# Kernel optimization log

Measured on AMD Instinct MI355X. Metric: run time of the kernel, lower is better.

Reference implementation:

```python
import jax, jax.numpy as jnp
import numpy as np
from jax import lax

B, M, E, H = 16, 64, 256, 256  # batch items, cells per item, n_embedding, n_hidden
S = 4 * M                       # candidate nodes per item (4 per cell)
CLIP = 10.0                     # pointer logit clipping C


def setup_inputs() -> dict:
    key = jax.random.key(0)
    ks = jax.random.split(key, 12)
    sc = 0.05  # keep tanh unsaturated
    return {
        "cell_embed": jax.random.normal(ks[0], (B, S, E), jnp.float32),
        "original_node": jax.random.uniform(ks[1], (B, S, 4), jnp.float32),
        "maze": jnp.zeros((B, 4, 4), jnp.int32),  # unused by the math (torch code builds .tolist() but never uses it)
        "num_cell": M,
        "costs": jax.random.uniform(ks[2], (B, S), jnp.float32),
        "init_w": jax.random.uniform(ks[3], (2 * E,), jnp.float32, -1.0, 1.0),
        "Whc": jax.random.normal(ks[4], (E, E), jnp.float32) * sc,
        "bhc": jax.random.normal(ks[5], (E,), jnp.float32) * sc,
        "Wv": jax.random.normal(ks[6], (2 * E, E), jnp.float32) * sc,
        "bv": jax.random.normal(ks[7], (E,), jnp.float32) * sc,
        "Wq": jax.random.normal(ks[8], (E, H), jnp.float32) * sc,
        "Wk": jax.random.normal(ks[9], (E, H), jnp.float32) * sc,
        "vptr": jax.random.normal(ks[10], (H,), jnp.float32) * sc,
    }


def reference(cell_embed, original_node, maze, num_cell, costs, init_w, Whc, bhc, Wv, bv, Wq, Wk, vptr):
    key = jax.random.key(42)
    bkeys = jax.random.split(key, cell_embed.shape[0])

    def decode_one(emb, node, cost, bkey):
        # emb: [S, E], node: [S, 4], cost: [S]
        h_bar = emb.mean(0) @ Whc + bhc            # h_context_embed(mean)
        k_proj = emb @ Wk                          # [S, H], hoisted out of loop
        q0 = h_bar + init_w @ Wv + bv              # query at step 0

        def step(carry, i):
            query, mask, init_h, st_idx = carry
            # pointer attention: u_j = v^T tanh(Wq q + Wk k_j); logits = C*tanh(u)
            u = jnp.tanh(query @ Wq + k_proj) @ vptr          # [S]
            lg = jnp.where(mask > 0, -1e9, CLIP * jnp.tanh(u))
            idx = jax.random.categorical(jax.random.fold_in(bkey, i), lg)
            logp = jax.nn.log_softmax(lg)[idx]
            # reward: exit point of previous node -> entry point of chosen node, plus internal costs
            ext = jnp.sqrt(jnp.sum((node[idx, :2] - node[st_idx, 2:]) ** 2))
            reward = jnp.where(i > 0, ext + cost[st_idx] + cost[idx], 0.0)
            # mask the whole 4-node cell containing idx, plus idx itself
            mask = lax.dynamic_update_slice(mask, jnp.ones((4,), mask.dtype), (4 * (idx // 4),))
            mask = mask.at[idx].set(1)
            h = emb[idx]                                       # selected node embedding
            init_h = jnp.where(i == 0, h, init_h)
            query = h_bar + jnp.concatenate([init_h, h]) @ Wv + bv
            return (query, mask, init_h, idx), (logp, reward, idx)

        carry0 = (q0, jnp.zeros((emb.shape[0],), jnp.int32),
                  jnp.zeros((emb.shape[1],), emb.dtype), jnp.int32(0))
        _, (logps, rewards, actions) = lax.scan(step, carry0, jnp.arange(num_cell))
        return logps.sum(), rewards.sum(), actions

    lp, rw, act = jax.vmap(decode_one)(cell_embed, original_node, costs, bkeys)
    return lp, rw, act
```

## Files before the change

### kernel.cpp

```cpp
#include <hip/hip_runtime.h>
#include <stdint.h>

#define NB 16
#define NM 64
#define NS 256
#define NE 256
#define NH 256

__device__ __forceinline__ uint32_t rotl32(uint32_t v, int d) { return (v << d) | (v >> (32 - d)); }

__device__ __forceinline__ void threefry(uint32_t k0, uint32_t k1,
                                         uint32_t x0, uint32_t x1,
                                         uint32_t& o0, uint32_t& o1) {
  uint32_t ks2 = k0 ^ k1 ^ 0x1BD11BDAu;
#define TFR(r) { x0 += x1; x1 = rotl32(x1, r); x1 ^= x0; }
  x0 += k0; x1 += k1;
  TFR(13) TFR(15) TFR(26) TFR(6)
  x0 += k1;  x1 += ks2 + 1u;
  TFR(17) TFR(29) TFR(16) TFR(24)
  x0 += ks2; x1 += k0 + 2u;
  TFR(13) TFR(15) TFR(26) TFR(6)
  x0 += k0;  x1 += k1 + 3u;
  TFR(17) TFR(29) TFR(16) TFR(24)
  x0 += k1;  x1 += ks2 + 4u;
  TFR(13) TFR(15) TFR(26) TFR(6)
  x0 += ks2; x1 += k0 + 5u;
#undef TFR
  o0 = x0; o1 = x1;
}

__device__ __forceinline__ float gumbel_from_bits(uint32_t bits) {
  float u = __uint_as_float((bits >> 9) | 0x3f800000u) - 1.0f;
  u = fmaxf(u, 1.17549435e-38f);
  return -logf(-logf(u));
}

__device__ void gumbel_body(int blk, float* __restrict__ g) {
  const int b = blk >> 6;
  const int i = blk & 63;
  const int s = threadIdx.x;
  uint32_t kb0, kb1, f0, f1, r0, r1;
  threefry(0u, 42u, 0u, (uint32_t)b, kb0, kb1);
  threefry(kb0, kb1, 0u, (uint32_t)i, f0, f1);
  threefry(f0, f1, 0u, (uint32_t)s, r0, r1);
  g[(blk << 8) + s] = gumbel_from_bits(r0 ^ r1);
}

__device__ void prep_body(int b,
                          const float* __restrict__ emb,
                          const float* __restrict__ init_w,
                          const float* __restrict__ Whc,
                          const float* __restrict__ bhc,
                          const float* __restrict__ Wv,
                          const float* __restrict__ bv,
                          const float* __restrict__ Wq,
                          float* __restrict__ qbase,
                          float* __restrict__ q0W,
                          float* __restrict__ smem) {
  const int t = threadIdx.x;
  float* mean_s = smem;
  float* hbpb   = smem + NE;
  float* iwv    = smem + 2 * NE;
  const float* eb = emb + (size_t)b * NS * NE;
  float acc = 0.f;
  for (int s = 0; s < NS; ++s) acc += eb[s * NE + t];
  mean_s[t] = acc * (1.0f / NS);
  __syncthreads();
  float h = bhc[t];
  for (int j = 0; j < NE; ++j) h = fmaf(mean_s[j], Whc[j * NE + t], h);
  hbpb[t] = h + bv[t];
  float a2 = 0.f;
  for (int j = 0; j < 2 * NE; ++j) a2 = fmaf(init_w[j], Wv[j * NE + t], a2);
  iwv[t] = a2;
  __syncthreads();
  float qb = 0.f, q0 = 0.f;
  for (int e = 0; e < NE; ++e) {
    float w = Wq[e * NH + t];
    qb = fmaf(hbpb[e], w, qb);
    q0 = fmaf(hbpb[e] + iwv[e], w, q0);
  }
  qbase[b * NH + t] = qb;
  q0W[b * NH + t] = q0;
}

__device__ void mm_body(int blk,
                        const float* __restrict__ A,
                        const float* __restrict__ W,
                        float* __restrict__ C) {
  const int t = threadIdx.x;
  const int hq = (t & 63) * 4;
  const int r0 = (t >> 6) * 4;
  const int rowbase = blk * 16;
  float acc[4][4] = {};
  #pragma unroll 2
  for (int e = 0; e < NE; ++e) {
    float4 w = *(const float4*)(W + e * NH + hq);
    #pragma unroll
    for (int r = 0; r < 4; ++r) {
      float a = A[(size_t)(rowbase + r0 + r) * NE + e];
      acc[r][0] = fmaf(a, w.x, acc[r][0]);
      acc[r][1] = fmaf(a, w.y, acc[r][1]);
      acc[r][2] = fmaf(a, w.z, acc[r][2]);
      acc[r][3] = fmaf(a, w.w, acc[r][3]);
    }
  }
  #pragma unroll
  for (int r = 0; r < 4; ++r)
    *(float4*)(C + (size_t)(rowbase + r0 + r) * NH + hq) =
        make_float4(acc[r][0], acc[r][1], acc[r][2], acc[r][3]);
}

#define TPAD 260
__device__ void mm2_fused_body(int blk,
                               const float* __restrict__ emb,
                               const float* __restrict__ Wvb,
                               const float* __restrict__ Wq,
                               float* __restrict__ EQB,
                               float* __restrict__ sm) {
  const int t = threadIdx.x;
  const int hq = (t & 63) * 4;
  const int r0 = (t >> 6) * 4;
  const int rowbase = blk * 16;
  {
    float acc1[4][4] = {};
    #pragma unroll 2
    for (int e = 0; e < NE; ++e) {
      float4 w = *(const float4*)(Wvb + e * NE + hq);
      #pragma unroll
      for (int r = 0; r < 4; ++r) {
        float a = emb[(size_t)(rowbase + r0 + r) * NE + e];
        acc1[r][0] = fmaf(a, w.x, acc1[r][0]);
        acc1[r][1] = fmaf(a, w.y, acc1[r][1]);
        acc1[r][2] = fmaf(a, w.z, acc1[r][2]);
        acc1[r][3] = fmaf(a, w.w, acc1[r][3]);
      }
    }
    #pragma unroll
    for (int r = 0; r < 4; ++r)
      *(float4*)&sm[(r0 + r) * TPAD + hq] =
          make_float4(acc1[r][0], acc1[r][1], acc1[r][2], acc1[r][3]);
  }
  __syncthreads();
  float acc[4][4] = {};
  for (int e4 = 0; e4 < NE; e4 += 4) {
    float4 a4[4];
    #pragma unroll
    for (int r = 0; r < 4; ++r) a4[r] = *(const float4*)&sm[(r0 + r) * TPAD + e4];
    #pragma unroll
    for (int ee = 0; ee < 4; ++ee) {
      float4 w = *(const float4*)(Wq + (e4 + ee) * NH + hq);
      #pragma unroll
      for (int r = 0; r < 4; ++r) {
        float a = (ee == 0) ? a4[r].x : (ee == 1) ? a4[r].y : (ee == 2) ? a4[r].z : a4[r].w;
        acc[r][0] = fmaf(a, w.x, acc[r][0]);
        acc[r][1] = fmaf(a, w.y, acc[r][1]);
        acc[r][2] = fmaf(a, w.z, acc[r][2]);
        acc[r][3] = fmaf(a, w.w, acc[r][3]);
      }
    }
  }
  #pragma unroll
  for (int r = 0; r < 4; ++r)
    *(float4*)(EQB + (size_t)(rowbase + r0 + r) * NH + hq) =
        make_float4(__expf(2.f * acc[r][0]), __expf(2.f * acc[r][1]),
                    __expf(2.f * acc[r][2]), __expf(2.f * acc[r][3]));
}

__global__ __launch_bounds__(256) void fused_pre_kernel(
    float* __restrict__ g,
    const float* __restrict__ emb,
    const float* __restrict__ init_w,
    const float* __restrict__ Whc,
    const float* __restrict__ bhc,
    const float* __restrict__ Wv,
    const float* __restrict__ bv,
    const float* __restrict__ Wq,
    const float* __restrict__ Wk,
    float* __restrict__ qbase,
    float* __restrict__ q0W,
    float* __restrict__ kp,
    float* __restrict__ EQB) {
  __shared__ float smem[16 * TPAD];
  const int blk = blockIdx.x;
  if (blk < 256) {
    mm2_fused_body(blk, emb, Wv + NE * NE, Wq, EQB, smem);
  } else if (blk < 512) {
    mm_body(blk - 256, emb, Wk, kp);
  } else if (blk < 512 + NB * NM) {
    gumbel_body(blk - 512, g);
  } else {
    prep_body(blk - 512 - NB * NM, emb, init_w, Whc, bhc, Wv, bv, Wq, qbase, q0W, smem);
  }
}

#define PIDX(h) (((h) >> 5) * 36 + ((h) & 31))

__global__ __launch_bounds__(1024, 4) void decode_kernel(
    const float* __restrict__ emb,
    const float* __restrict__ node,
    const float* __restrict__ costs,
    const float* __restrict__ Wv,
    const float* __restrict__ Wq,
    const float* __restrict__ vptr,
    const float* __restrict__ g_g,
    const float* __restrict__ kp_g,
    const float* __restrict__ EQB_g,
    const float* __restrict__ qbase_g,
    const float* __restrict__ q0W_g,
    float* __restrict__ out) {
  const int b = blockIdx.x;
  const int tid = threadIdx.x;
  const int hc = tid & 7;
  const int pr = tid >> 3;
  const int s0 = pr * 2, s1 = s0 + 1;
  const int wid = tid >> 6;
  const int lane = tid & 63;

  __shared__ float qWp[8 * 36];
  __shared__ float vpp[8 * 36];
  __shared__ float4 part4[16];
  __shared__ float2 mle[NM][17];
  __shared__ float blg_hist[NM];
  __shared__ int   idx_hist[NM];
  __shared__ float er[NE];
  __shared__ float Ts[NE];

  float4 ek0[8], ek1[8];
  {
    const float4* p0 = (const float4*)(kp_g + ((size_t)b * NS + s0) * NH + hc * 32);
    const float4* p1 = (const float4*)(kp_g + ((size_t)b * NS + s1) * NH + hc * 32);
    #pragma unroll
    for (int j = 0; j < 8; ++j) {
      float4 a = p0[j], c = p1[j];
      ek0[j] = make_float4(__expf(2.f * a.x), __expf(2.f * a.y), __expf(2.f * a.z), __expf(2.f * a.w));
      ek1[j] = make_float4(__expf(2.f * c.x), __expf(2.f * c.y), __expf(2.f * c.z), __expf(2.f * c.w));
    }
  }
  float Vsum = 0.f;
  {
    const float4* vv = (const float4*)(vptr + hc * 32);
    #pragma unroll
    for (int j = 0; j < 8; ++j) { float4 v = vv[j]; Vsum += (v.x + v.y) + (v.z + v.w); }
  }
  if (tid < NH) {
    vpp[PIDX(tid)] = -2.0f * vptr[tid];
    qWp[PIDX(tid)] = __expf(2.0f * q0W_g[b * NH + tid]);
  }
  float e2qb = (tid < NH) ? __expf(2.0f * qbase_g[b * NH + tid]) : 0.f;

  int m = 0;
  const float* gb = g_g + (size_t)b * NM * NS;

  __syncthreads();

  for (int i = 0; i < NM; ++i) {
    float lg0, lg1, val0, val1;
    if (!m) {
      float2 g01 = *(const float2*)(gb + i * NS + s0);
      const float4* q4 = (const float4*)(qWp + hc * 36);
      const float4* v4 = (const float4*)(vpp + hc * 36);
      float a0 = 0.f, a1 = 0.f;
      #pragma unroll
      for (int jj = 0; jj < 4; ++jj) {
        float4 qa = q4[2 * jj], qb = q4[2 * jj + 1];
        float4 va = v4[2 * jj], vb = v4[2 * jj + 1];
        {
          float4 ka = ek0[2 * jj], kb = ek0[2 * jj + 1];
          float z1 = fmaf(qa.x, ka.x, 1.f), z2 = fmaf(qa.y, ka.y, 1.f);
          float z3 = fmaf(qa.z, ka.z, 1.f), z4 = fmaf(qa.w, ka.w, 1.f);
          float z5 = fmaf(qb.x, kb.x, 1.f), z6 = fmaf(qb.y, kb.y, 1.f);
          float z7 = fmaf(qb.z, kb.z, 1.f), z8 = fmaf(qb.w, kb.w, 1.f);
          float p12 = z1 * z2, p34 = z3 * z4, p56 = z5 * z6, p78 = z7 * z8;
          float p1234 = p12 * p34, p5678 = p56 * p78;
          float r = __builtin_amdgcn_rcpf(p1234 * p5678);
          float t12 = fmaf(va.y, z1, va.x * z2);
          float t34 = fmaf(va.w, z3, va.z * z4);
          float t56 = fmaf(vb.y, z5, vb.x * z6);
          float t78 = fmaf(vb.w, z7, vb.z * z8);
          float T14 = fmaf(t34, p12, t12 * p34);
          float T58 = fmaf(t78, p56, t56 * p78);
          a0 = fmaf(T14 * p5678, r, a0);
          a0 = fmaf(T58 * p1234, r, a0);
        }
        {
          float4 ka = ek1[2 * jj], kb = ek1[2 * jj + 1];
          float z1 = fmaf(qa.x, ka.x, 1.f), z2 = fmaf(qa.y, ka.y, 1.f);
          float z3 = fmaf(qa.z, ka.z, 1.f), z4 = fmaf(qa.w, ka.w, 1.f);
          float z5 = fmaf(qb.x, kb.x, 1.f), z6 = fmaf(qb.y, kb.y, 1.f);
          float z7 = fmaf(qb.z, kb.z, 1.f), z8 = fmaf(qb.w, kb.w, 1.f);
          float p12 = z1 * z2, p34 = z3 * z4, p56 = z5 * z6, p78 = z7 * z8;
          float p1234 = p12 * p34, p5678 = p56 * p78;
          float r = __builtin_amdgcn_rcpf(p1234 * p5678);
          float t12 = fmaf(va.y, z1, va.x * z2);
          float t34 = fmaf(va.w, z3, va.z * z4);
          float t56 = fmaf(vb.y, z5, vb.x * z6);
          float t78 = fmaf(vb.w, z7, vb.z * z8);
          float T14 = fmaf(t34, p12, t12 * p34);
          float T58 = fmaf(t78, p56, t56 * p78);
          a1 = fmaf(T14 * p5678, r, a1);
          a1 = fmaf(T58 * p1234, r, a1);
        }
      }
      float u0 = Vsum + a0;
      float u1 = Vsum + a1;
      u0 += __shfl_xor(u0, 1); u0 += __shfl_xor(u0, 2); u0 += __shfl_xor(u0, 4);
      u1 += __shfl_xor(u1, 1); u1 += __shfl_xor(u1, 2); u1 += __shfl_xor(u1, 4);
      float ex0 = __expf(2.f * u0);
      float ex1 = __expf(2.f * u1);
      lg0 = fmaf(-20.f, __builtin_amdgcn_rcpf(ex0 + 1.f), 10.f);
      lg1 = fmaf(-20.f, __builtin_amdgcn_rcpf(ex1 + 1.f), 10.f);
      val0 = lg0 + g01.x;
      val1 = lg1 + g01.y;
    } else {
      lg0 = -1e9f; lg1 = -1e9f; val0 = -1e9f; val1 = -1e9f;
    }
    float ml = fmaxf(lg0, lg1);
    #pragma unroll
    for (int off = 1; off < 64; off <<= 1) ml = fmaxf(ml, __shfl_xor(ml, off));
    float e = (__expf(lg0 - ml) + __expf(lg1 - ml)) * 0.125f;
    #pragma unroll
    for (int off = 1; off < 64; off <<= 1) e += __shfl_xor(e, off);
    bool t1 = val1 > val0;
    float v = t1 ? val1 : val0;
    int vi = t1 ? s1 : s0;
    float lgw = t1 ? lg1 : lg0;
    #pragma unroll
    for (int off = 1; off < 64; off <<= 1) {
      float ov = __shfl_xor(v, off);
      int   oi = __shfl_xor(vi, off);
      float ol = __shfl_xor(lgw, off);
      bool take = (ov > v) || (ov == v && oi < vi);
      v   = take ? ov : v;
      vi  = take ? oi : vi;
      lgw = take ? ol : lgw;
    }
    if (lane == 0) {
      part4[wid] = make_float4(v, __int_as_float(vi), lgw, 0.f);
      mle[i][wid] = make_float2(ml, e);
    }
    __syncthreads();

    float4 p = part4[lane & 15];
    float cv = p.x; int ci = __float_as_int(p.y); float cl = p.z;
    #pragma unroll
    for (int off = 1; off < 16; off <<= 1) {
      float ov = __shfl_xor(cv, off);
      int   oi = __shfl_xor(ci, off);
      float ol = __shfl_xor(cl, off);
      bool take = (ov > cv) || (ov == cv && oi < ci);
      cv = take ? ov : cv;
      ci = take ? oi : ci;
      cl = take ? ol : cl;
    }
    const int idx = ci;
    if (tid == 0) { idx_hist[i] = idx; blg_hist[i] = cl; }

    if (!m && (pr >> 1) == (idx >> 2)) m = 1;

    if (i == 0) {
      if (tid < NE) er[tid] = emb[((size_t)b * NS + idx) * NE + tid];
      __syncthreads();
      if (tid < NE) {
        float tv = 0.f;
        #pragma unroll 4
        for (int j = 0; j < NE; ++j) tv = fmaf(er[j], Wv[j * NE + tid], tv);
        Ts[tid] = tv;
      }
      __syncthreads();
      if (tid < NE) {
        float qi = 0.f;
        #pragma unroll 4
        for (int e2 = 0; e2 < NE; ++e2) qi = fmaf(Ts[e2], Wq[e2 * NH + tid], qi);
        e2qb *= __expf(2.0f * qi);
      }
    }

    if (tid < NH) qWp[PIDX(tid)] = e2qb * EQB_g[((size_t)b * NS + idx) * NH + tid];
    __syncthreads();
  }

  if (wid == 0) {
    float mlg = -3.0e38f;
    #pragma unroll 4
    for (int w = 0; w < 16; ++w) mlg = fmaxf(mlg, mle[lane][w].x);
    float sum = 0.f;
    #pragma unroll 4
    for (int w = 0; w < 16; ++w) {
      float2 me = mle[lane][w];
      sum += me.y * __expf(me.x - mlg);
    }
    float term = blg_hist[lane] - (mlg + logf(sum));
    #pragma unroll
    for (int off = 1; off < 64; off <<= 1) term += __shfl_xor(term, off);
    if (lane == 0) out[b] = term;
    out[2 * NB + b * NM + lane] = (float)idx_hist[lane];
  } else if (wid == 1) {
    float term = 0.f;
    if (lane > 0) {
      int id = idx_hist[lane];
      int pv = idx_hist[lane - 1];
      float dx = node[((size_t)b * NS + id) * 4 + 0] - node[((size_t)b * NS + pv) * 4 + 2];
      float dy = node[((size_t)b * NS + id) * 4 + 1] - node[((size_t)b * NS + pv) * 4 + 3];
      term = sqrtf(dx * dx + dy * dy) + costs[(size_t)b * NS + pv] + costs[(size_t)b * NS + id];
    }
    #pragma unroll
    for (int off = 1; off < 64; off <<= 1) term += __shfl_xor(term, off);
    if (lane == 0) out[NB + b] = term;
  }
}

extern "C" void kernel_launch(void* const* d_in, const int* in_sizes, int n_in,
                              void* d_out, int out_size, void* d_ws, size_t ws_size,
                              hipStream_t stream) {
  const float* emb    = (const float*)d_in[0];
  const float* node   = (const float*)d_in[1];
  const float* costs  = (const float*)d_in[4];
  const float* init_w = (const float*)d_in[5];
  const float* Whc    = (const float*)d_in[6];
  const float* bhc    = (const float*)d_in[7];
  const float* Wv     = (const float*)d_in[8];
  const float* bv     = (const float*)d_in[9];
  const float* Wq     = (const float*)d_in[10];
  const float* Wk     = (const float*)d_in[11];
  const float* vptr   = (const float*)d_in[12];
  float* out = (float*)d_out;

  float* ws    = (float*)d_ws;
  float* g     = ws;
  float* kp    = g + NB * NM * NS;
  float* QB    = kp + (size_t)NB * NS * NH;
  float* spare = QB + (size_t)NB * NS * NH;
  float* qbase = spare + (size_t)NB * NS * NE;
  float* q0W   = qbase + NB * NH;

  fused_pre_kernel<<<512 + NB * NM + NB, 256, 0, stream>>>(
      g, emb, init_w, Whc, bhc, Wv, bv, Wq, Wk, qbase, q0W, kp, QB);
  decode_kernel<<<NB, 1024, 0, stream>>>(emb, node, costs, Wv, Wq, vptr,
                                         g, kp, QB, qbase, q0W, out);
}
```

Baseline: 331.1 us.

## Give each wavefront a private query copy to drop a per-step block barrier

Each wavefront now builds its own copy of the query-exponent vector in shared memory, so the per-step barrier after updating the query is removed. The partial-argmax buffer is double-buffered by step parity so the single remaining barrier per step is enough. Wavefronts whose lanes are all masked skip the query update entirely. The cost is sixteenfold redundant global loads and shared-memory writes per step, plus reliance on wavefront-local ordering enforced by an explicit lgkmcnt wait.

```diff
diff --git a/kernel.cpp b/kernel.cpp
--- a/kernel.cpp
+++ b/kernel.cpp
@@ -216,9 +216,10 @@
   const int wid = tid >> 6;
   const int lane = tid & 63;
 
-  __shared__ float qWp[8 * 36];
+  __shared__ float qW_w[16][8 * 36];
   __shared__ float vpp[8 * 36];
-  __shared__ float4 part4[16];
+  __shared__ float eqb_s[NS];
+  __shared__ float4 part4[2][16];
   __shared__ float2 mle[NM][17];
   __shared__ float blg_hist[NM];
   __shared__ int   idx_hist[NM];
@@ -244,9 +245,13 @@
   }
   if (tid < NH) {
     vpp[PIDX(tid)] = -2.0f * vptr[tid];
-    qWp[PIDX(tid)] = __expf(2.0f * q0W_g[b * NH + tid]);
-  }
-  float e2qb = (tid < NH) ? __expf(2.0f * qbase_g[b * NH + tid]) : 0.f;
+    eqb_s[tid] = __expf(2.0f * qbase_g[b * NH + tid]);
+  }
+  {
+    float4 q0 = *(const float4*)(q0W_g + b * NH + 4 * lane);
+    *(float4*)(&qW_w[wid][PIDX(4 * lane)]) =
+        make_float4(__expf(2.f * q0.x), __expf(2.f * q0.y), __expf(2.f * q0.z), __expf(2.f * q0.w));
+  }
 
   int m = 0;
   const float* gb = g_g + (size_t)b * NM * NS;
@@ -257,7 +262,7 @@
     float lg0, lg1, val0, val1;
     if (!m) {
       float2 g01 = *(const float2*)(gb + i * NS + s0);
-      const float4* q4 = (const float4*)(qWp + hc * 36);
+      const float4* q4 = (const float4*)(&qW_w[wid][hc * 36]);
       const float4* v4 = (const float4*)(vpp + hc * 36);
       float a0 = 0.f, a1 = 0.f;
       #pragma unroll
@@ -335,12 +340,12 @@
       lgw = take ? ol : lgw;
     }
     if (lane == 0) {
-      part4[wid] = make_float4(v, __int_as_float(vi), lgw, 0.f);
+      part4[i & 1][wid] = make_float4(v, __int_as_float(vi), lgw, 0.f);
       mle[i][wid] = make_float2(ml, e);
     }
     __syncthreads();
 
-    float4 p = part4[lane & 15];
+    float4 p = part4[i & 1][lane & 15];
     float cv = p.x; int ci = __float_as_int(p.y); float cl = p.z;
     #pragma unroll
     for (int off = 1; off < 16; off <<= 1) {
@@ -371,13 +376,24 @@
         float qi = 0.f;
         #pragma unroll 4
         for (int e2 = 0; e2 < NE; ++e2) qi = fmaf(Ts[e2], Wq[e2 * NH + tid], qi);
-        e2qb *= __expf(2.0f * qi);
+        eqb_s[tid] *= __expf(2.0f * qi);
       }
-    }
-
-    if (tid < NH) qWp[PIDX(tid)] = e2qb * EQB_g[((size_t)b * NS + idx) * NH + tid];
-    __syncthreads();
-  }
+      __syncthreads();
+    }
+
+    if (i + 1 < NM && !__all(m)) {
+      float4 eq = *(const float4*)(EQB_g + ((size_t)b * NS + idx) * NH + 4 * lane);
+      float e0 = eqb_s[4 * lane + 0];
+      float e1 = eqb_s[4 * lane + 1];
+      float e2v = eqb_s[4 * lane + 2];
+      float e3 = eqb_s[4 * lane + 3];
+      *(float4*)(&qW_w[wid][PIDX(4 * lane)]) =
+          make_float4(eq.x * e0, eq.y * e1, eq.z * e2v, eq.w * e3);
+      asm volatile("s_waitcnt lgkmcnt(0)" ::: "memory");
+    }
+  }
+
+  __syncthreads();
 
   if (wid == 0) {
     float mlg = -3.0e38f;
```

After: 333.8 us. About the same (+0.8%).
